# Performance work log

Hardware: AMD Instinct MI355X
Metric: run time of the kernel (lower is better)

## Reference

```python
import jax, jax.numpy as jnp
import numpy as np

B, LQ, LS, S = 64, 64, 512, 512
NEG = -1e6


def mask_for_lengths(lengths, max_len, mask_right=True):
    pos = jnp.arange(max_len)
    if mask_right:
        m = pos[None, :] >= lengths[:, None]
    else:
        m = pos[None, :] < lengths[:, None]
    return jnp.where(m, jnp.float32(NEG), jnp.float32(0.0))


def setup_inputs() -> dict:
    key = jax.random.key(0)
    ks = jax.random.split(key, 12)
    f = lambda k, shp: jax.random.normal(k, shp, jnp.float32)
    sc = np.float32(1.0 / np.sqrt(S))
    return {
        "encoded_question": f(ks[0], (B, LQ, S)),
        "encoded_support": f(ks[1], (B, LS, S)),
        "question_length": jax.random.randint(ks[2], (B,), 1, LQ + 1),
        "support_length": jax.random.randint(ks[3], (B,), LS // 2, LS + 1),
        "correct_start": jax.random.randint(ks[4], (B,), 0, LS),
        "answer2question": jnp.arange(B),
        "is_eval": 1,
        "W_qa": f(ks[5], (S, 1)) * sc,
        "W_qsi": f(ks[6], (S, S)) * sc,
        "b_qsi": jnp.zeros((S,), jnp.float32),
        "W_qs": f(ks[7], (2 * S, S)) * sc,
        "W_ss": f(ks[8], (S, 1)) * sc,
        "W_qei": f(ks[9], (S, S)) * sc,
        "b_qei": jnp.zeros((S,), jnp.float32),
        "W_qe": f(ks[10], (3 * S, S)) * sc,
        "W_es": f(ks[11], (S, 1)) * sc,
    }


def reference(encoded_question, encoded_support, question_length, support_length,
              correct_start, answer2question, is_eval,
              W_qa, W_qsi, b_qsi, W_qs, W_ss, W_qei, b_qei, W_qe, W_es):
    # question attention pooling
    att = jnp.einsum('bqd,do->bq', encoded_question, W_qa)
    att = att + mask_for_lengths(question_length, LQ)
    w = jax.nn.softmax(att, axis=1)                                   # [B,LQ]
    q_state = jnp.einsum('bqd,bq->bd', encoded_question, w)           # [B,S]

    # start scoring
    start_input = jnp.concatenate(
        [q_state[:, None, :] * encoded_support, encoded_support], axis=2)  # [B,LS,2S]
    q_start_inter = q_state @ W_qsi + b_qsi                           # [B,S]
    q_start_state = start_input @ W_qs + q_start_inter[:, None, :]    # [B,LS,S]
    support_mask = mask_for_lengths(support_length, LS)
    start_scores = jnp.einsum('bld,do->bl', jax.nn.relu(q_start_state), W_ss)
    start_scores = start_scores + support_mask                        # [B,LS]
    predicted_start_pointer = jnp.argmax(start_scores, axis=1)        # [B]

    # eval path: start_pointer = predicted argmax
    start_pointer = predicted_start_pointer
    u_s = jnp.take_along_axis(encoded_support,
                              start_pointer[:, None, None], axis=1)[:, 0, :]  # [B,S]

    # end scoring
    end_input = jnp.concatenate(
        [encoded_support * u_s[:, None, :], start_input], axis=2)     # [B,LS,3S]
    q_end_inter = q_state @ W_qei + b_qei
    q_end_state = end_input @ W_qe + q_end_inter[:, None, :]          # [B,LS,S]
    end_scores = jnp.einsum('bld,do->bl', jax.nn.relu(q_end_state), W_es)
    end_scores = end_scores + support_mask
    # eval: mask positions left of start_pointer
    end_scores = end_scores + mask_for_lengths(start_pointer, LS, mask_right=False)
    predicted_end_pointer = jnp.argmax(end_scores, axis=1)

    return (start_scores, end_scores, predicted_start_pointer, predicted_end_pointer)
```

## Files before the change

### kernel.cpp

```cpp
#include <hip/hip_runtime.h>
#include <math.h>

constexpr int B_  = 64;
constexpr int LQ_ = 64;
constexpr int LS_ = 512;
constexpr int S_  = 512;
#define NEGV (-1e6f)
#define MARGIN 0.0625f

typedef __attribute__((ext_vector_type(8))) short bf16x8;
typedef __attribute__((ext_vector_type(4))) float f32x4;

__device__ inline unsigned short f2bf_rn(float x) {
    unsigned u = __builtin_bit_cast(unsigned, x);
    unsigned r = (u + 0x7FFFu + ((u >> 16) & 1u)) >> 16;
    return (unsigned short)r;
}

__global__ __launch_bounds__(512)
void qpool_inter_kernel(const float* __restrict__ eq, const int* __restrict__ qlen,
                        const float* __restrict__ W_qa,
                        const float* __restrict__ W_qsi, const float* __restrict__ b_qsi,
                        const float* __restrict__ W_qei, const float* __restrict__ b_qei,
                        float* __restrict__ q_state,
                        float* __restrict__ qsi, float* __restrict__ qei)
{
    int b = blockIdx.x;
    int which = blockIdx.y;
    const float* W  = which ? W_qei : W_qsi;
    const float* bi = which ? b_qei : b_qsi;
    float*       o  = which ? qei   : qsi;

    int t = threadIdx.x, lane = t & 63, w = t >> 6;
    __shared__ float att[LQ_], wsm[LQ_], qs[S_];
    __shared__ float red[8][S_];
    const float* eqb = eq + (size_t)b * LQ_ * S_;

    #pragma unroll
    for (int k = 0; k < 8; ++k) {
        int q = w + 8 * k;
        const float* row = eqb + q * S_;
        float s = 0.f;
        #pragma unroll
        for (int j = 0; j < 8; ++j)
            s = fmaf(row[lane + 64 * j], W_qa[lane + 64 * j], s);
        #pragma unroll
        for (int off = 32; off >= 1; off >>= 1)
            s += __shfl_xor(s, off);
        if (lane == 0) att[q] = s;
    }
    __syncthreads();

    if (w == 0) {
        int L = qlen[b];
        float v = att[lane] + ((lane < L) ? 0.f : NEGV);
        float m = v;
        #pragma unroll
        for (int off = 32; off >= 1; off >>= 1)
            m = fmaxf(m, __shfl_xor(m, off));
        float e = expf(v - m);
        float sum = e;
        #pragma unroll
        for (int off = 32; off >= 1; off >>= 1)
            sum += __shfl_xor(sum, off);
        wsm[lane] = e / sum;
    }
    __syncthreads();

    {
        float acc = 0.f;
        #pragma unroll 8
        for (int q = 0; q < LQ_; ++q)
            acc = fmaf(wsm[q], eqb[q * S_ + t], acc);
        qs[t] = acc;
        if (which == 0) q_state[b * S_ + t] = acc;
    }
    __syncthreads();

    {
        float z[8];
        #pragma unroll
        for (int k = 0; k < 8; ++k) z[k] = 0.f;
        const int d0 = w * 64;
        #pragma unroll 4
        for (int dd = 0; dd < 64; ++dd) {
            int d = d0 + dd;
            float q = qs[d];
            const float* row = W + (size_t)d * S_ + lane;
            #pragma unroll
            for (int k = 0; k < 8; ++k)
                z[k] = fmaf(q, row[k * 64], z[k]);
        }
        #pragma unroll
        for (int k = 0; k < 8; ++k) red[w][k * 64 + lane] = z[k];
    }
    __syncthreads();
    {
        float acc = bi[t];
        #pragma unroll
        for (int ww = 0; ww < 8; ++ww) acc += red[ww][t];
        o[b * S_ + t] = acc;
    }
}

__device__ inline int select_cands(const float* s_l, int t, int lane, int w,
                                   float* wred, int* wcnt, int* cand)
{
    float v = s_l[t];
    #pragma unroll
    for (int off = 32; off >= 1; off >>= 1)
        v = fmaxf(v, __shfl_xor(v, off));
    if (lane == 0) wred[w] = v;
    __syncthreads();
    float m = wred[0];
    #pragma unroll
    for (int k = 1; k < 8; ++k) m = fmaxf(m, wred[k]);
    float th = m - MARGIN;
    bool flag = s_l[t] >= th;
    unsigned long long bal = __ballot(flag);
    int rank = __popcll(bal & ((1ull << lane) - 1ull));
    if (lane == 0) wcnt[w] = (int)__popcll(bal);
    __syncthreads();
    int off = 0, total = 0;
    #pragma unroll
    for (int k = 0; k < 8; ++k) { if (k < w) off += wcnt[k]; total += wcnt[k]; }
    if (flag) { int pos = off + rank; if (pos < 8) cand[pos] = t; }
    __syncthreads();
    return total < 8 ? total : 8;
}

__global__ __launch_bounds__(512)
void prep_start_kernel(const float* __restrict__ W, const float* __restrict__ q_state,
                       short* __restrict__ Wc)
{
    int bid = blockIdx.x;
    int i = bid >> 6, b = bid & 63;
    int col = threadIdx.x;
    __shared__ float scq[32];
    if (col < 32) scq[col] = q_state[b * S_ + i * 32 + col];
    __syncthreads();

    unsigned short h[32];
    #pragma unroll
    for (int d = 0; d < 32; ++d) {
        int D = i * 32 + d;
        float v = fmaf(scq[d], W[(size_t)D * S_ + col], W[(size_t)(S_ + D) * S_ + col]);
        h[d] = f2bf_rn(v);
    }
    size_t base = (size_t)b * 262144 + (size_t)i * 16384 + (size_t)col * 8;
    #pragma unroll
    for (int kc = 0; kc < 4; ++kc) {
        uint4 H;
        H.x = h[kc*8+0] | ((unsigned)h[kc*8+1] << 16);
        H.y = h[kc*8+2] | ((unsigned)h[kc*8+3] << 16);
        H.z = h[kc*8+4] | ((unsigned)h[kc*8+5] << 16);
        H.w = h[kc*8+6] | ((unsigned)h[kc*8+7] << 16);
        *(uint4*)&Wc[base + kc * 4096] = H;
    }
}

__global__ __launch_bounds__(512)
void prep_end_kernel(const float* __restrict__ W, const float* __restrict__ q_state,
                     const float* __restrict__ es, const float* __restrict__ start_scores,
                     const float* __restrict__ part,
                     int* __restrict__ sp_ws, float* __restrict__ pred_start,
                     short* __restrict__ Wc)
{
    int bid = blockIdx.x;
    int i = bid >> 6, b = bid & 63;
    int t = threadIdx.x, lane = t & 63, w = t >> 6;
    __shared__ float s_l[S_];
    __shared__ float wred[8];
    __shared__ int wcnt[8], cand[8];
    __shared__ float scq[32], scu[32];
    __shared__ int best_sh;

    s_l[t] = start_scores[b * S_ + t];
    __syncthreads();
    int cnt = select_cands(s_l, t, lane, w, wred, wcnt, cand);

    if (t == 0) {
        int bi = cand[0];
        if (cnt > 1) {
            float bv = -INFINITY;
            for (int c = 0; c < cnt; ++c) {
                float e = part[b * 8 + c];
                if (e > bv) { bv = e; bi = cand[c]; }
            }
        }
        best_sh = bi;
        if (i == 0) { pred_start[b] = (float)bi; sp_ws[b] = bi; }
    }
    __syncthreads();
    int best = best_sh;

    if (t < 32) scq[t] = q_state[b * S_ + i * 32 + t];
    if (t >= 32 && t < 64)
        scu[t - 32] = es[((size_t)(b * LS_ + best)) * S_ + i * 32 + (t - 32)];
    __syncthreads();

    int col = t;
    unsigned short h[32];
    #pragma unroll
    for (int d = 0; d < 32; ++d) {
        int D = i * 32 + d;
        float v = fmaf(scu[d], W[(size_t)D * S_ + col],
                  fmaf(scq[d], W[(size_t)(S_ + D) * S_ + col],
                       W[(size_t)(2 * S_ + D) * S_ + col]));
        h[d] = f2bf_rn(v);
    }
    size_t base = (size_t)b * 262144 + (size_t)i * 16384 + (size_t)col * 8;
    #pragma unroll
    for (int kc = 0; kc < 4; ++kc) {
        uint4 H;
        H.x = h[kc*8+0] | ((unsigned)h[kc*8+1] << 16);
        H.y = h[kc*8+2] | ((unsigned)h[kc*8+3] << 16);
        H.z = h[kc*8+4] | ((unsigned)h[kc*8+5] << 16);
        H.w = h[kc*8+6] | ((unsigned)h[kc*8+7] << 16);
        *(uint4*)&Wc[base + kc * 4096] = H;
    }
}

template <bool END>
__global__ __launch_bounds__(512)
void score_kernel(const float* __restrict__ es, const short* __restrict__ Wc,
                  const float* __restrict__ inter, const float* __restrict__ Wsmall,
                  const int* __restrict__ slen, const int* __restrict__ sp,
                  float* __restrict__ out)
{
    const int t = threadIdx.x;
    const int lane = t & 63, wid = t >> 6;
    const int wr = wid >> 2, wc = wid & 3;
    const int l15 = lane & 15, l4 = lane >> 4;

    int lid = blockIdx.x;
    int xcd = lid & 7, slot = lid >> 3;
    int b  = xcd * 8 + (slot >> 2);
    int rc = slot & 3;

    __shared__ __attribute__((aligned(16))) short As3[3][4096];
    __shared__ __attribute__((aligned(16))) short Bs3[3][16384];
    __shared__ float int_l[S_], wsm_l[S_];
    __shared__ float sm_red[128][4];

    int_l[t] = inter[b * S_ + t];
    wsm_l[t] = Wsmall[t];

    const char* Bbase = (const char*)(Wc + (size_t)b * 262144);

    f32x4 acc[4][8];
    #pragma unroll
    for (int r = 0; r < 4; ++r)
        #pragma unroll
        for (int c = 0; c < 8; ++c)
            acc[r][c] = (f32x4){0.f, 0.f, 0.f, 0.f};

    const int arow = t >> 2, akc = t & 3;
    const float* aptr = es + ((size_t)(b * LS_ + rc * 128 + arow)) * S_ + akc * 8;

    auto stageB = [&](int i, int buf) {
        const char* gb = Bbase + (size_t)i * 32768 + t * 16;
        char* lb = (char*)Bs3[buf] + t * 16;
        #pragma unroll
        for (int q = 0; q < 4; ++q)
            __builtin_amdgcn_global_load_lds(
                (const __attribute__((address_space(1))) void*)(gb + q * 8192),
                (__attribute__((address_space(3))) void*)(lb + q * 8192), 16, 0, 0);
    };
    auto buildA = [&](int buf, float4 a0, float4 a1) {
        uint4 HA;
        HA.x = f2bf_rn(a0.x) | ((unsigned)f2bf_rn(a0.y) << 16);
        HA.y = f2bf_rn(a0.z) | ((unsigned)f2bf_rn(a0.w) << 16);
        HA.z = f2bf_rn(a1.x) | ((unsigned)f2bf_rn(a1.y) << 16);
        HA.w = f2bf_rn(a1.z) | ((unsigned)f2bf_rn(a1.w) << 16);
        *(uint4*)&As3[buf][akc * 1024 + arow * 8] = HA;
    };

    float4 a0 = *(const float4*)(aptr);
    float4 a1 = *(const float4*)(aptr + 4);
    stageB(0, 0);
    stageB(1, 1);

    for (int i = 0; i < 16; ++i) {
        const int buf = i % 3;

        float4 n0 = {0,0,0,0}, n1 = {0,0,0,0};
        if (i + 1 < 16) {
            n0 = *(const float4*)(aptr + (i + 1) * 32);
            n1 = *(const float4*)(aptr + (i + 1) * 32 + 4);
        }
        if (i + 2 < 16) stageB(i + 2, (i + 2) % 3);

        buildA(buf, a0, a1);
        a0 = n0; a1 = n1;

        if (i + 2 < 16)      asm volatile("s_waitcnt vmcnt(10) lgkmcnt(0)" ::: "memory");
        else if (i + 1 < 16) asm volatile("s_waitcnt vmcnt(6) lgkmcnt(0)" ::: "memory");
        else                 asm volatile("s_waitcnt vmcnt(0) lgkmcnt(0)" ::: "memory");
        __builtin_amdgcn_s_barrier();

        bf16x8 ah[4];
        #pragma unroll
        for (int r = 0; r < 4; ++r) {
            int rowp = wr * 64 + r * 16 + l15;
            ah[r] = *(const bf16x8*)&As3[buf][l4 * 1024 + rowp * 8];
        }
        #pragma unroll
        for (int c = 0; c < 8; ++c) {
            int col = wc * 128 + c * 16 + l15;
            bf16x8 bh = *(const bf16x8*)&Bs3[buf][l4 * 4096 + col * 8];
            #pragma unroll
            for (int r = 0; r < 4; ++r)
                acc[r][c] = __builtin_amdgcn_mfma_f32_16x16x32_bf16(ah[r], bh, acc[r][c], 0, 0, 0);
        }
        asm volatile("s_waitcnt lgkmcnt(0)" ::: "memory");
        __builtin_amdgcn_s_barrier();
    }

    #pragma unroll
    for (int r = 0; r < 4; ++r) {
        #pragma unroll
        for (int jj = 0; jj < 4; ++jj) {
            float pr = 0.f;
            #pragma unroll
            for (int c = 0; c < 8; ++c) {
                int col = wc * 128 + c * 16 + l15;
                float v = acc[r][c][jj] + int_l[col];
                v = fmaxf(v, 0.f);
                pr = fmaf(v, wsm_l[col], pr);
            }
            pr += __shfl_xor(pr, 1);
            pr += __shfl_xor(pr, 2);
            pr += __shfl_xor(pr, 4);
            pr += __shfl_xor(pr, 8);
            if (l15 == 0) sm_red[wr * 64 + r * 16 + l4 * 4 + jj][wc] = pr;
        }
    }
    __syncthreads();
    if (t < 128) {
        int l = rc * 128 + t;
        float s = sm_red[t][0] + sm_red[t][1] + sm_red[t][2] + sm_red[t][3];
        if (l >= slen[b]) s += NEGV;
        if (END) { if (l < sp[b]) s += NEGV; }
        out[b * LS_ + l] = s;
    }
}

template <bool END>
__global__ __launch_bounds__(512)
void rescue_kernel(const float* __restrict__ support, const float* __restrict__ q_state,
                   const int* __restrict__ sp, const float* __restrict__ Wbig,
                   const float* __restrict__ inter, const float* __restrict__ Wsmall,
                   const float* __restrict__ scores, float* __restrict__ part)
{
    int bid = blockIdx.x;
    int b = bid >> 3, cslot = bid & 7;
    int t = threadIdx.x, lane = t & 63, w = t >> 6;
    __shared__ float s_l[S_], qs_l[S_], us_l[S_], arow_sh[S_];
    __shared__ float red[8][S_];
    __shared__ float wred[8];
    __shared__ int wcnt[8], cand[8];

    s_l[t]  = scores[b * S_ + t];
    qs_l[t] = q_state[b * S_ + t];
    if (END) {
        int spv = sp[b];
        us_l[t] = support[((size_t)(b * LS_ + spv)) * S_ + t];
    }
    __syncthreads();

    int cnt = select_cands(s_l, t, lane, w, wred, wcnt, cand);
    if (cnt == 1 || cslot >= cnt) return;

    int ci = cand[cslot];
    arow_sh[t] = support[((size_t)(b * LS_ + ci)) * S_ + t];
    __syncthreads();

    const float* W1 = Wbig;
    const float* W2 = Wbig + (size_t)S_ * S_;
    const float* W3 = Wbig + (size_t)2 * S_ * S_;
    const int d0 = w * 64;

    float z[8];
    #pragma unroll
    for (int j = 0; j < 8; ++j) z[j] = 0.f;

    #pragma unroll 2
    for (int dd = 0; dd < 64; ++dd) {
        int d = d0 + dd;
        float a  = arow_sh[d];
        float qa = qs_l[d] * a;
        float ua = END ? us_l[d] * a : 0.f;
        const float* r1 = W1 + (size_t)d * S_ + lane;
        const float* r2 = W2 + (size_t)d * S_ + lane;
        const float* r3 = W3 + (size_t)d * S_ + lane;
        #pragma unroll
        for (int j = 0; j < 8; ++j) {
            if (END)
                z[j] = fmaf(ua, r1[64 * j], fmaf(qa, r2[64 * j], fmaf(a, r3[64 * j], z[j])));
            else
                z[j] = fmaf(qa, r1[64 * j], fmaf(a, r2[64 * j], z[j]));
        }
    }
    #pragma unroll
    for (int j = 0; j < 8; ++j) red[w][lane + 64 * j] = z[j];
    __syncthreads();

    float v = 0.f;
    #pragma unroll
    for (int ww = 0; ww < 8; ++ww) v += red[ww][t];
    float p = fmaxf(v + inter[b * S_ + t], 0.f) * Wsmall[t];
    #pragma unroll
    for (int off = 32; off >= 1; off >>= 1)
        p += __shfl_xor(p, off);
    if (lane == 0) wred[w] = p;
    __syncthreads();
    if (t == 0) {
        float e = ((wred[0] + wred[1]) + (wred[2] + wred[3])) +
                  ((wred[4] + wred[5]) + (wred[6] + wred[7]));
        part[b * 8 + cslot] = e;
    }
}

__global__ __launch_bounds__(512)
void finalize_end_kernel(const float* __restrict__ scores, const float* __restrict__ part,
                         float* __restrict__ pred)
{
    int b = blockIdx.x;
    int t = threadIdx.x, lane = t & 63, w = t >> 6;
    __shared__ float s_l[S_];
    __shared__ float wred[8];
    __shared__ int wcnt[8], cand[8];

    s_l[t] = scores[b * S_ + t];
    __syncthreads();
    int cnt = select_cands(s_l, t, lane, w, wred, wcnt, cand);

    if (t == 0) {
        int bi = cand[0];
        if (cnt > 1) {
            float bv = -INFINITY;
            for (int c = 0; c < cnt; ++c) {
                float e = part[b * 8 + c];
                if (e > bv) { bv = e; bi = cand[c]; }
            }
        }
        pred[b] = (float)bi;
    }
}

extern "C" void kernel_launch(void* const* d_in, const int* in_sizes, int n_in,
                              void* d_out, int out_size, void* d_ws, size_t ws_size,
                              hipStream_t stream)
{
    const float* eq    = (const float*)d_in[0];
    const float* es    = (const float*)d_in[1];
    const int*   qlen  = (const int*)d_in[2];
    const int*   slen  = (const int*)d_in[3];
    const float* W_qa  = (const float*)d_in[7];
    const float* W_qsi = (const float*)d_in[8];
    const float* b_qsi = (const float*)d_in[9];
    const float* W_qs  = (const float*)d_in[10];
    const float* W_ss  = (const float*)d_in[11];
    const float* W_qei = (const float*)d_in[12];
    const float* b_qei = (const float*)d_in[13];
    const float* W_qe  = (const float*)d_in[14];
    const float* W_es  = (const float*)d_in[15];

    float* out          = (float*)d_out;
    float* start_scores = out;
    float* end_scores   = out + B_ * LS_;
    float* pred_start   = out + 2 * B_ * LS_;
    float* pred_end     = out + 2 * B_ * LS_ + B_;

    float* ws      = (float*)d_ws;
    float* q_state = ws;
    float* qsi     = ws + B_ * S_;
    float* qei     = ws + 2 * B_ * S_;
    float* part    = ws + 3 * B_ * S_;
    int*   sp_ws   = (int*)(ws + 3 * B_ * S_ + 512);
    short* Wc      = (short*)(ws + 3 * B_ * S_ + 1024);

    qpool_inter_kernel<<<dim3(B_, 2), 512, 0, stream>>>(
        eq, qlen, W_qa, W_qsi, b_qsi, W_qei, b_qei, q_state, qsi, qei);

    prep_start_kernel<<<1024, 512, 0, stream>>>(W_qs, q_state, Wc);
    score_kernel<false><<<256, 512, 0, stream>>>(es, Wc, qsi, W_ss, slen, nullptr, start_scores);
    rescue_kernel<false><<<B_ * 8, 512, 0, stream>>>(es, q_state, nullptr, W_qs, qsi, W_ss,
                                                     start_scores, part);

    prep_end_kernel<<<1024, 512, 0, stream>>>(W_qe, q_state, es, start_scores, part,
                                              sp_ws, pred_start, Wc);
    score_kernel<true><<<256, 512, 0, stream>>>(es, Wc, qei, W_es, slen, sp_ws, end_scores);
    rescue_kernel<true><<<B_ * 8, 512, 0, stream>>>(es, q_state, sp_ws, W_qe, qei, W_es,
                                                    end_scores, part);
    finalize_end_kernel<<<B_, 512, 0, stream>>>(end_scores, part, pred_end);
}
```

Baseline: 166.0 us.

## Stream fp32 A tiles to LDS via async loads, convert to bf16 at fragment read

The activation (A) tile used to be loaded into registers, converted to bf16 and written to LDS by each thread, with loads issued one stage ahead. It is now copied as fp32 straight into a triple-buffered, XOR-swizzled LDS tile with global_load_lds, alongside the B tile, and converted to bf16 when the MFMA fragments are read. This takes register staging and LDS store instructions off the critical path and lets A prefetch two stages ahead. In exchange, the A LDS buffer doubles in size, which may reduce occupancy, and every wave repeats the conversion work for shared rows.

Result: slower. 172.1 us (+3.6%).

```diff
diff --git a/kernel.cpp b/kernel.cpp
--- a/kernel.cpp
+++ b/kernel.cpp
@@ -238,7 +238,7 @@
     int b  = xcd * 8 + (slot >> 2);
     int rc = slot & 3;
 
-    __shared__ __attribute__((aligned(16))) short As3[3][4096];
+    __shared__ __attribute__((aligned(16))) float Asf[3][4096];
     __shared__ __attribute__((aligned(16))) short Bs3[3][16384];
     __shared__ float int_l[S_], wsm_l[S_];
     __shared__ float sm_red[128][4];
@@ -246,6 +246,7 @@
     int_l[t] = inter[b * S_ + t];
     wsm_l[t] = Wsmall[t];
 
+    const char* esb   = (const char*)(es + ((size_t)(b * LS_ + rc * 128)) * S_);
     const char* Bbase = (const char*)(Wc + (size_t)b * 262144);
 
     f32x4 acc[4][8];
@@ -255,10 +256,19 @@
         for (int c = 0; c < 8; ++c)
             acc[r][c] = (f32x4){0.f, 0.f, 0.f, 0.f};
 
-    const int arow = t >> 2, akc = t & 3;
-    const float* aptr = es + ((size_t)(b * LS_ + rc * 128 + arow)) * S_ + akc * 8;
-
-    auto stageB = [&](int i, int buf) {
+    const int arow = t >> 3, aslot = t & 7;
+    const int acc_sw = aslot ^ (arow & 7);
+
+    auto stage = [&](int i, int buf) {
+        const char* ga0 = esb + (size_t)arow * 2048 + (size_t)i * 128 + acc_sw * 16;
+        const char* ga1 = ga0 + (size_t)64 * 2048;
+        char* la = (char*)Asf[buf] + t * 16;
+        __builtin_amdgcn_global_load_lds(
+            (const __attribute__((address_space(1))) void*)ga0,
+            (__attribute__((address_space(3))) void*)la, 16, 0, 0);
+        __builtin_amdgcn_global_load_lds(
+            (const __attribute__((address_space(1))) void*)ga1,
+            (__attribute__((address_space(3))) void*)(la + 8192), 16, 0, 0);
         const char* gb = Bbase + (size_t)i * 32768 + t * 16;
         char* lb = (char*)Bs3[buf] + t * 16;
         #pragma unroll
@@ -267,43 +277,34 @@
                 (const __attribute__((address_space(1))) void*)(gb + q * 8192),
                 (__attribute__((address_space(3))) void*)(lb + q * 8192), 16, 0, 0);
     };
-    auto buildA = [&](int buf, float4 a0, float4 a1) {
-        uint4 HA;
-        HA.x = f2bf_rn(a0.x) | ((unsigned)f2bf_rn(a0.y) << 16);
-        HA.y = f2bf_rn(a0.z) | ((unsigned)f2bf_rn(a0.w) << 16);
-        HA.z = f2bf_rn(a1.x) | ((unsigned)f2bf_rn(a1.y) << 16);
-        HA.w = f2bf_rn(a1.z) | ((unsigned)f2bf_rn(a1.w) << 16);
-        *(uint4*)&As3[buf][akc * 1024 + arow * 8] = HA;
-    };
-
-    float4 a0 = *(const float4*)(aptr);
-    float4 a1 = *(const float4*)(aptr + 4);
-    stageB(0, 0);
-    stageB(1, 1);
+
+    stage(0, 0);
+    stage(1, 1);
 
     for (int i = 0; i < 16; ++i) {
         const int buf = i % 3;
-
-        float4 n0 = {0,0,0,0}, n1 = {0,0,0,0};
-        if (i + 1 < 16) {
-            n0 = *(const float4*)(aptr + (i + 1) * 32);
-            n1 = *(const float4*)(aptr + (i + 1) * 32 + 4);
-        }
-        if (i + 2 < 16) stageB(i + 2, (i + 2) % 3);
-
-        buildA(buf, a0, a1);
-        a0 = n0; a1 = n1;
-
-        if (i + 2 < 16)      asm volatile("s_waitcnt vmcnt(10) lgkmcnt(0)" ::: "memory");
-        else if (i + 1 < 16) asm volatile("s_waitcnt vmcnt(6) lgkmcnt(0)" ::: "memory");
-        else                 asm volatile("s_waitcnt vmcnt(0) lgkmcnt(0)" ::: "memory");
+        if (i + 2 < 16) stage(i + 2, (i + 2) % 3);
+
+        if (i + 2 < 16)      asm volatile("s_waitcnt vmcnt(12)" ::: "memory");
+        else if (i + 1 < 16) asm volatile("s_waitcnt vmcnt(6)" ::: "memory");
+        else                 asm volatile("s_waitcnt vmcnt(0)" ::: "memory");
         __builtin_amdgcn_s_barrier();
 
         bf16x8 ah[4];
         #pragma unroll
         for (int r = 0; r < 4; ++r) {
             int rowp = wr * 64 + r * 16 + l15;
-            ah[r] = *(const bf16x8*)&As3[buf][l4 * 1024 + rowp * 8];
+            int s0 = (2 * l4) ^ (rowp & 7);
+            int s1 = (2 * l4 + 1) ^ (rowp & 7);
+            const char* rbase = (const char*)Asf[buf] + rowp * 128;
+            float4 f0 = *(const float4*)(rbase + s0 * 16);
+            float4 f1 = *(const float4*)(rbase + s1 * 16);
+            bf16x8 hv;
+            hv[0] = (short)f2bf_rn(f0.x); hv[1] = (short)f2bf_rn(f0.y);
+            hv[2] = (short)f2bf_rn(f0.z); hv[3] = (short)f2bf_rn(f0.w);
+            hv[4] = (short)f2bf_rn(f1.x); hv[5] = (short)f2bf_rn(f1.y);
+            hv[6] = (short)f2bf_rn(f1.z); hv[7] = (short)f2bf_rn(f1.w);
+            ah[r] = hv;
         }
         #pragma unroll
         for (int c = 0; c < 8; ++c) {
```
